# Optimization experiments

Hardware: AMD Instinct MI355X
Metric: run time of the kernel (lower is better)

The kernel has to match this reference:

```python
import jax, jax.numpy as jnp
import numpy as np

D_MODEL = 1024
N_HEADS = 16
D_HEAD = D_MODEL // N_HEADS
SCALE = D_HEAD ** -0.5


def setup_inputs() -> dict:
    key = jax.random.key(0)
    ks = jax.random.split(key, 9)
    s = 0.02
    x = jax.random.normal(ks[0], (2, 2048, D_MODEL), dtype=jnp.float32)
    Wq = jax.random.normal(ks[1], (D_MODEL, D_MODEL), dtype=jnp.float32) * s
    Wk = jax.random.normal(ks[2], (D_MODEL, D_MODEL), dtype=jnp.float32) * s
    Wv = jax.random.normal(ks[3], (D_MODEL, D_MODEL), dtype=jnp.float32) * s
    Wo = jax.random.normal(ks[4], (D_MODEL, D_MODEL), dtype=jnp.float32) * s
    bq = jax.random.normal(ks[5], (D_MODEL,), dtype=jnp.float32) * s
    bk = jax.random.normal(ks[6], (D_MODEL,), dtype=jnp.float32) * s
    bv = jax.random.normal(ks[7], (D_MODEL,), dtype=jnp.float32) * s
    bo = jax.random.normal(ks[8], (D_MODEL,), dtype=jnp.float32) * s
    return {"x": x, "Wq": Wq, "bq": bq, "Wk": Wk, "bk": bk,
            "Wv": Wv, "bv": bv, "Wo": Wo, "bo": bo}


def reference(x, Wq, bq, Wk, bk, Wv, bv, Wo, bo):
    B, S, _ = x.shape
    # torch nn.Linear: y = x @ W.T + b
    def proj(W, b):
        h = jnp.einsum('bsd,ed->bse', x, W) + b
        return h.reshape(B, S, N_HEADS, D_HEAD).transpose(0, 2, 1, 3)  # [B,H,S,Dh]
    Q = proj(Wq, bq)
    K = proj(Wk, bk)
    V = proj(Wv, bv)
    # chunked QK^T softmax over full K == full attention (no mask, dropout=0)
    scores = jnp.einsum('bhqd,bhkd->bhqk', Q, K) * SCALE  # [B,H,S,S]
    attn = jax.nn.softmax(scores, axis=-1)
    out = jnp.einsum('bhqk,bhkd->bhqd', attn, V)
    out = out.transpose(0, 2, 1, 3).reshape(B, S, D_MODEL)
    return jnp.einsum('bsd,ed->bse', out, Wo) + bo
```

## Files before the change

kernel.cpp:

```cpp
#include <hip/hip_runtime.h>
#include <cstdint>
#include <cstddef>


typedef unsigned short u16;
typedef unsigned int u32;
typedef __bf16 bf16x8 __attribute__((ext_vector_type(8)));
typedef float f32x4 __attribute__((ext_vector_type(4)));

#define GLOAD_LDS16(gp, lp)                                                            \
  __builtin_amdgcn_global_load_lds((const __attribute__((address_space(1))) void*)(gp),\
                                   (__attribute__((address_space(3))) void*)(lp),      \
                                   16, 0, 0)

__device__ __forceinline__ u16 f2bf(float f) {
  unsigned u = __builtin_bit_cast(unsigned, f);
  u = u + 0x7fffu + ((u >> 16) & 1u);
  return (u16)(u >> 16);
}

__device__ __forceinline__ u32 pack_bf2(float a, float b) {
  u32 ua = __builtin_bit_cast(u32, a) + 0x8000u;
  u32 ub = __builtin_bit_cast(u32, b) + 0x8000u;
  return __builtin_amdgcn_perm(ub, ua, 0x07060302u);
}

#define QSCALE 0.1803368801111204f

__global__ void cvt_all(const float* __restrict__ x,
                        const float* __restrict__ wq, const float* __restrict__ wk,
                        const float* __restrict__ wv, const float* __restrict__ wo,
                        u16* __restrict__ xb, u16* __restrict__ wqb,
                        u16* __restrict__ wkb, u16* __restrict__ wvb,
                        u16* __restrict__ wob) {
  int bx = blockIdx.x;
  const float* s; u16* d; int off;
  if (bx < 2048)      { s = x;  d = xb;  off = bx; }
  else if (bx < 2560) { s = wq; d = wqb; off = bx - 2048; }
  else if (bx < 3072) { s = wk; d = wkb; off = bx - 2560; }
  else if (bx < 3584) { s = wv; d = wvb; off = bx - 3072; }
  else                { s = wo; d = wob; off = bx - 3584; }
  int i = off * 2048 + threadIdx.x * 8;
  float4 a = *(const float4*)(s + i);
  float4 b = *(const float4*)(s + i + 4);
  uint4 o;
  o.x = f2bf(a.x) | ((u32)f2bf(a.y) << 16);
  o.y = f2bf(a.z) | ((u32)f2bf(a.w) << 16);
  o.z = f2bf(b.x) | ((u32)f2bf(b.y) << 16);
  o.w = f2bf(b.z) | ((u32)f2bf(b.w) << 16);
  *(uint4*)(d + i) = o;
}

template <int MODE>
__global__ __launch_bounds__(256, 3) void gemm_mfma(
    const u16* __restrict__ A,
    const u16* __restrict__ W0, const u16* __restrict__ W1, const u16* __restrict__ W2,
    const float* __restrict__ b0, const float* __restrict__ b1, const float* __restrict__ b2,
    u16* __restrict__ o0, u16* __restrict__ o1, u16* __restrict__ o2,
    float* __restrict__ oF)
{
  __shared__ __align__(16) u16 As[128 * 64];
  __shared__ __align__(16) u16 Bs[128 * 64];

  const int tid = threadIdx.x;
  const int w = tid >> 6, l = tid & 63;
  const int lane = l & 15, quad = l >> 4;
  const int wm = w >> 1, wn = w & 1;
  const int m0 = blockIdx.y * 128;
  const int n0g = blockIdx.x * 128;

  const int src = (MODE == 0) ? (n0g >> 10) : 0;
  const u16* Wsel = (MODE == 0) ? (src == 0 ? W0 : (src == 1 ? W1 : W2)) : W0;
  const float* bsel = (MODE == 0) ? (src == 0 ? b0 : (src == 1 ? b1 : b2)) : b0;
  const int n_base = (MODE == 0) ? (n0g & 1023) : n0g;

  const int c8 = ((l & 7) ^ (l >> 3)) * 8;

  f32x4 acc[4][4] = {};

  for (int kt = 0; kt < 1024; kt += 64) {
    __syncthreads();
    const u16* Ag = A + (size_t)m0 * 1024 + kt;
    const u16* Bg = Wsel + (size_t)n_base * 1024 + kt;
    #pragma unroll
    for (int i = 0; i < 4; ++i) {
      int rr = w * 32 + i * 8;
      GLOAD_LDS16(Ag + (size_t)(rr + (l >> 3)) * 1024 + c8, As + rr * 64);
      GLOAD_LDS16(Bg + (size_t)(rr + (l >> 3)) * 1024 + c8, Bs + rr * 64);
    }
    __syncthreads();

    bf16x8 af[4][2], bf[4][2];
    #pragma unroll
    for (int mf = 0; mf < 4; ++mf)
      #pragma unroll
      for (int ks = 0; ks < 2; ++ks) {
        af[mf][ks] = *(const bf16x8*)((const char*)As +
            (wm * 64 + mf * 16 + lane) * 128 + (((ks * 4 + quad) ^ (lane & 7)) * 16));
        bf[mf][ks] = *(const bf16x8*)((const char*)Bs +
            (wn * 64 + mf * 16 + lane) * 128 + (((ks * 4 + quad) ^ (lane & 7)) * 16));
      }
    #pragma unroll
    for (int ks = 0; ks < 2; ++ks)
      #pragma unroll
      for (int mf = 0; mf < 4; ++mf)
        #pragma unroll
        for (int nf = 0; nf < 4; ++nf)
          acc[mf][nf] = __builtin_amdgcn_mfma_f32_16x16x32_bf16(
              af[mf][ks], bf[nf][ks], acc[mf][nf], 0, 0, 0);
  }

  float bb[4];
  #pragma unroll
  for (int nf = 0; nf < 4; ++nf) bb[nf] = bsel[n_base + wn * 64 + nf * 16 + lane];

  u16* osel = (MODE == 0) ? (src == 0 ? o0 : (src == 1 ? o1 : o2)) : o0;

  #pragma unroll
  for (int mf = 0; mf < 4; ++mf) {
    int mb = m0 + wm * 64 + mf * 16 + quad * 4;
    #pragma unroll
    for (int nf = 0; nf < 4; ++nf) {
      int n_l = wn * 64 + nf * 16 + lane;
      if (MODE == 0 && src == 2) {
        float v0 = acc[mf][nf][0] + bb[nf];
        float v1 = acc[mf][nf][1] + bb[nf];
        float v2 = acc[mf][nf][2] + bb[nf];
        float v3 = acc[mf][nf][3] + bb[nf];
        int bi = mb >> 11, s = mb & 2047;
        int n_in = n_base + n_l;
        int h = n_in >> 6, dh = n_in & 63;
        uint2 pk = make_uint2(pack_bf2(v0, v1), pack_bf2(v2, v3));
        *(uint2*)(osel + (((size_t)(bi * 16 + h) * 64 + dh) * 2048 + s)) = pk;
      } else {
        #pragma unroll
        for (int r = 0; r < 4; ++r) {
          float v = acc[mf][nf][r] + bb[nf];
          int m = mb + r;
          if (MODE == 0) {
            if (src == 0) v *= QSCALE;
            int bi = m >> 11, s = m & 2047;
            int n_in = n_base + n_l;
            int h = n_in >> 6, dh = n_in & 63;
            osel[(((size_t)(bi * 16 + h) * 2048 + s) << 6) + dh] = f2bf(v);
          } else {
            oF[(size_t)m * 1024 + n0g + n_l] = v;
          }
        }
      }
    }
  }
}

__global__ __launch_bounds__(256, 2) void attn_mfma(
    const u16* __restrict__ Qg_, const u16* __restrict__ Kg_,
    const u16* __restrict__ VTg_, u16* __restrict__ Og)
{
  __shared__ __align__(16) u16 Ks[2][64 * 64];
  __shared__ __align__(16) u16 Vs[2][64 * 64];
  __shared__ __align__(16) u16 Ps[4][32 * 64];

  const int tid = threadIdx.x;
  const int w = tid >> 6, l = tid & 63;
  const int lane = l & 15, quad = l >> 4;
  const int bh = blockIdx.y;
  const int q0 = blockIdx.x * 128;

  const u16* Qg = Qg_ + ((size_t)bh * 2048 + q0) * 64;
  const u16* Kg = Kg_ + (size_t)bh * 2048 * 64;
  const u16* VTg = VTg_ + (size_t)bh * 64 * 2048;

  const int c8 = ((l & 7) ^ (l >> 3)) * 8;
  const int lrow = l >> 3;

  bf16x8 bq[2][2];
  #pragma unroll
  for (int qf = 0; qf < 2; ++qf)
    #pragma unroll
    for (int ks = 0; ks < 2; ++ks)
      bq[qf][ks] = *(const bf16x8*)(Qg +
          (size_t)(w * 32 + qf * 16 + lane) * 64 + ks * 32 + quad * 8);

  #pragma unroll
  for (int i = 0; i < 2; ++i) {
    int rr = w * 16 + i * 8;
    GLOAD_LDS16(Kg + (size_t)(rr + lrow) * 64 + c8, Ks[0] + rr * 64);
    GLOAD_LDS16(VTg + (size_t)(rr + lrow) * 2048 + c8, Vs[0] + rr * 64);
  }

  f32x4 oa[2][4] = {};
  float lsum[2] = {0.f, 0.f};
  u16* Pw = Ps[w];

  for (int kt = 0; kt < 32; ++kt) {
    const int buf = kt & 1;
    __syncthreads();
    if (kt < 31) {
      const u16* Kt = Kg + (size_t)(kt + 1) * 64 * 64;
      const u16* Vt = VTg + (size_t)(kt + 1) * 64;
      #pragma unroll
      for (int i = 0; i < 2; ++i) {
        int rr = w * 16 + i * 8;
        GLOAD_LDS16(Kt + (size_t)(rr + lrow) * 64 + c8, Ks[buf ^ 1] + rr * 64);
        GLOAD_LDS16(Vt + (size_t)(rr + lrow) * 2048 + c8, Vs[buf ^ 1] + rr * 64);
      }
    }

    f32x4 sa[4][2] = {};
    #pragma unroll
    for (int ks = 0; ks < 2; ++ks)
      #pragma unroll
      for (int kf = 0; kf < 4; ++kf) {
        bf16x8 ak = *(const bf16x8*)((const char*)Ks[buf] +
            (kf * 16 + lane) * 128 + (((ks * 4 + quad) ^ (lane & 7)) * 16));
        #pragma unroll
        for (int qf = 0; qf < 2; ++qf)
          sa[kf][qf] = __builtin_amdgcn_mfma_f32_16x16x32_bf16(
              ak, bq[qf][ks], sa[kf][qf], 0, 0, 0);
      }

    #pragma unroll
    for (int qf = 0; qf < 2; ++qf) {
      int qrow = qf * 16 + lane;
      #pragma unroll
      for (int kf = 0; kf < 4; ++kf) {
        float p0 = __builtin_amdgcn_exp2f(sa[kf][qf][0]);
        float p1 = __builtin_amdgcn_exp2f(sa[kf][qf][1]);
        float p2 = __builtin_amdgcn_exp2f(sa[kf][qf][2]);
        float p3 = __builtin_amdgcn_exp2f(sa[kf][qf][3]);
        lsum[qf] += (p0 + p1) + (p2 + p3);
        int c = kf * 2 + (quad >> 1);
        *(uint2*)((char*)Pw + qrow * 128 + ((c ^ (lane & 7)) * 16) + (quad & 1) * 8)
            = make_uint2(pack_bf2(p0, p1), pack_bf2(p2, p3));
      }
    }

    #pragma unroll
    for (int ks = 0; ks < 2; ++ks) {
      bf16x8 bv[4];
      #pragma unroll
      for (int df = 0; df < 4; ++df)
        bv[df] = *(const bf16x8*)((const char*)Vs[buf] +
            (df * 16 + lane) * 128 + (((ks * 4 + quad) ^ (lane & 7)) * 16));
      #pragma unroll
      for (int qf = 0; qf < 2; ++qf) {
        bf16x8 ap = *(const bf16x8*)((const char*)Pw +
            (qf * 16 + lane) * 128 + (((ks * 4 + quad) ^ (lane & 7)) * 16));
        #pragma unroll
        for (int df = 0; df < 4; ++df)
          oa[qf][df] = __builtin_amdgcn_mfma_f32_16x16x32_bf16(
              ap, bv[df], oa[qf][df], 0, 0, 0);
      }
    }
  }

  #pragma unroll
  for (int qf = 0; qf < 2; ++qf) {
    lsum[qf] += __shfl_xor(lsum[qf], 16);
    lsum[qf] += __shfl_xor(lsum[qf], 32);
  }
  #pragma unroll
  for (int qf = 0; qf < 2; ++qf)
    #pragma unroll
    for (int r = 0; r < 4; ++r) {
      float inv = 1.0f / __shfl(lsum[qf], quad * 4 + r, 16);
      int qg = q0 + w * 32 + qf * 16 + quad * 4 + r;
      size_t base = ((size_t)(bh >> 4) * 2048 + qg) * 1024 + (bh & 15) * 64;
      #pragma unroll
      for (int df = 0; df < 4; ++df)
        Og[base + df * 16 + lane] = f2bf(oa[qf][df][r] * inv);
    }
}

extern "C" void kernel_launch(void* const* d_in, const int* in_sizes, int n_in,
                              void* d_out, int out_size, void* d_ws, size_t ws_size,
                              hipStream_t stream)
{
  (void)in_sizes; (void)n_in; (void)out_size; (void)ws_size;
  const float* x  = (const float*)d_in[0];
  const float* Wq = (const float*)d_in[1];
  const float* bq = (const float*)d_in[2];
  const float* Wk = (const float*)d_in[3];
  const float* bk = (const float*)d_in[4];
  const float* Wv = (const float*)d_in[5];
  const float* bv = (const float*)d_in[6];
  const float* Wo = (const float*)d_in[7];
  const float* bo = (const float*)d_in[8];
  float* y = (float*)d_out;

  const size_t NM = (size_t)4096 * 1024;
  u16* xb  = (u16*)d_ws;
  u16* wqb = xb + NM;
  u16* wkb = wqb + 1024 * 1024;
  u16* wvb = wkb + 1024 * 1024;
  u16* wob = wvb + 1024 * 1024;
  u16* Qb  = wob + 1024 * 1024;
  u16* Kb  = Qb + NM;
  u16* VTb = Kb + NM;
  u16* AOb = VTb + NM;

  cvt_all<<<4096, 256, 0, stream>>>(x, Wq, Wk, Wv, Wo, xb, wqb, wkb, wvb, wob);

  gemm_mfma<0><<<dim3(24, 32), 256, 0, stream>>>(
      xb, wqb, wkb, wvb, bq, bk, bv, Qb, Kb, VTb, nullptr);

  attn_mfma<<<dim3(16, 32), 256, 0, stream>>>(Qb, Kb, VTb, AOb);

  gemm_mfma<1><<<dim3(8, 32), 256, 0, stream>>>(
      AOb, wob, nullptr, nullptr, bo, nullptr, nullptr,
      nullptr, nullptr, nullptr, y);
}
```

Measured before the change: 191.6 us.

## Load K/V tiles directly into registers per wave, drop shared K/V staging

```diff
diff --git a/kernel.cpp b/kernel.cpp
--- a/kernel.cpp
+++ b/kernel.cpp
@@ -156,120 +156,118 @@
     const u16* __restrict__ Qg_, const u16* __restrict__ Kg_,
     const u16* __restrict__ VTg_, u16* __restrict__ Og)
 {
-  __shared__ __align__(16) u16 Ks[2][64 * 64];
-  __shared__ __align__(16) u16 Vs[2][64 * 64];
-  __shared__ __align__(16) u16 Ps[4][32 * 64];
+  __shared__ __align__(16) u16 Ps[4][32 * 72];
 
   const int tid = threadIdx.x;
   const int w = tid >> 6, l = tid & 63;
   const int lane = l & 15, quad = l >> 4;
   const int bh = blockIdx.y;
-  const int q0 = blockIdx.x * 128;
+  const int q0 = blockIdx.x * 128 + w * 32;
 
   const u16* Qg = Qg_ + ((size_t)bh * 2048 + q0) * 64;
-  const u16* Kg = Kg_ + (size_t)bh * 2048 * 64;
-  const u16* VTg = VTg_ + (size_t)bh * 64 * 2048;
-
-  const int c8 = ((l & 7) ^ (l >> 3)) * 8;
-  const int lrow = l >> 3;
+  const u16* Kg = Kg_ + (size_t)bh * 2048 * 64 + (size_t)lane * 64 + quad * 8;
+  const u16* VTg = VTg_ + (size_t)bh * 64 * 2048 + (size_t)lane * 2048 + quad * 8;
 
   bf16x8 bq[2][2];
   #pragma unroll
   for (int qf = 0; qf < 2; ++qf)
     #pragma unroll
     for (int ks = 0; ks < 2; ++ks)
-      bq[qf][ks] = *(const bf16x8*)(Qg +
-          (size_t)(w * 32 + qf * 16 + lane) * 64 + ks * 32 + quad * 8);
-
-  #pragma unroll
-  for (int i = 0; i < 2; ++i) {
-    int rr = w * 16 + i * 8;
-    GLOAD_LDS16(Kg + (size_t)(rr + lrow) * 64 + c8, Ks[0] + rr * 64);
-    GLOAD_LDS16(VTg + (size_t)(rr + lrow) * 2048 + c8, Vs[0] + rr * 64);
-  }
+      bq[qf][ks] = *(const bf16x8*)(Qg + (size_t)(qf * 16 + lane) * 64 + ks * 32 + quad * 8);
 
   f32x4 oa[2][4] = {};
   float lsum[2] = {0.f, 0.f};
   u16* Pw = Ps[w];
 
-  for (int kt = 0; kt < 32; ++kt) {
-    const int buf = kt & 1;
-    __syncthreads();
-    if (kt < 31) {
-      const u16* Kt = Kg + (size_t)(kt + 1) * 64 * 64;
-      const u16* Vt = VTg + (size_t)(kt + 1) * 64;
-      #pragma unroll
-      for (int i = 0; i < 2; ++i) {
-        int rr = w * 16 + i * 8;
-        GLOAD_LDS16(Kt + (size_t)(rr + lrow) * 64 + c8, Ks[buf ^ 1] + rr * 64);
-        GLOAD_LDS16(Vt + (size_t)(rr + lrow) * 2048 + c8, Vs[buf ^ 1] + rr * 64);
-      }
-    }
-
-    f32x4 sa[4][2] = {};
+  bf16x8 akA[4][2], akB[4][2];
+  #pragma unroll
+  for (int kf = 0; kf < 4; ++kf)
     #pragma unroll
     for (int ks = 0; ks < 2; ++ks)
-      #pragma unroll
-      for (int kf = 0; kf < 4; ++kf) {
-        bf16x8 ak = *(const bf16x8*)((const char*)Ks[buf] +
-            (kf * 16 + lane) * 128 + (((ks * 4 + quad) ^ (lane & 7)) * 16));
-        #pragma unroll
-        for (int qf = 0; qf < 2; ++qf)
-          sa[kf][qf] = __builtin_amdgcn_mfma_f32_16x16x32_bf16(
-              ak, bq[qf][ks], sa[kf][qf], 0, 0, 0);
-      }
-
-    #pragma unroll
-    for (int qf = 0; qf < 2; ++qf) {
-      int qrow = qf * 16 + lane;
-      #pragma unroll
-      for (int kf = 0; kf < 4; ++kf) {
-        float p0 = __builtin_amdgcn_exp2f(sa[kf][qf][0]);
-        float p1 = __builtin_amdgcn_exp2f(sa[kf][qf][1]);
-        float p2 = __builtin_amdgcn_exp2f(sa[kf][qf][2]);
-        float p3 = __builtin_amdgcn_exp2f(sa[kf][qf][3]);
-        lsum[qf] += (p0 + p1) + (p2 + p3);
-        int c = kf * 2 + (quad >> 1);
-        *(uint2*)((char*)Pw + qrow * 128 + ((c ^ (lane & 7)) * 16) + (quad & 1) * 8)
-            = make_uint2(pack_bf2(p0, p1), pack_bf2(p2, p3));
-      }
-    }
-
-    #pragma unroll
-    for (int ks = 0; ks < 2; ++ks) {
-      bf16x8 bv[4];
-      #pragma unroll
-      for (int df = 0; df < 4; ++df)
-        bv[df] = *(const bf16x8*)((const char*)Vs[buf] +
-            (df * 16 + lane) * 128 + (((ks * 4 + quad) ^ (lane & 7)) * 16));
-      #pragma unroll
-      for (int qf = 0; qf < 2; ++qf) {
-        bf16x8 ap = *(const bf16x8*)((const char*)Pw +
-            (qf * 16 + lane) * 128 + (((ks * 4 + quad) ^ (lane & 7)) * 16));
-        #pragma unroll
-        for (int df = 0; df < 4; ++df)
-          oa[qf][df] = __builtin_amdgcn_mfma_f32_16x16x32_bf16(
-              ap, bv[df], oa[qf][df], 0, 0, 0);
-      }
-    }
-  }
+      akA[kf][ks] = *(const bf16x8*)(Kg + (size_t)(kf * 16) * 64 + ks * 32);
+
+#define TILE_BODY(AKC, AKN, KT)                                                 \
+  {                                                                             \
+    const int kt_ = (KT);                                                       \
+           \
+    bf16x8 bv[4][2];                                                            \
+    _Pragma("unroll") for (int df = 0; df < 4; ++df)                            \
+      _Pragma("unroll") for (int ks = 0; ks < 2; ++ks)                          \
+        bv[df][ks] = *(const bf16x8*)(VTg + (size_t)df * 32768 + kt_ * 64 + ks * 32); \
+         \
+    f32x4 sa[4][2] = {};                                                        \
+    _Pragma("unroll") for (int ks = 0; ks < 2; ++ks)                            \
+      _Pragma("unroll") for (int kf = 0; kf < 4; ++kf)                          \
+        _Pragma("unroll") for (int qf = 0; qf < 2; ++qf)                        \
+          sa[kf][qf] = __builtin_amdgcn_mfma_f32_16x16x32_bf16(                 \
+              AKC[kf][ks], bq[qf][ks], sa[kf][qf], 0, 0, 0);                    \
+                   \
+    {                                                                           \
+      int ktn = kt_ + 1; if (ktn > 31) ktn = 31;                                \
+      _Pragma("unroll") for (int kf = 0; kf < 4; ++kf)                          \
+        _Pragma("unroll") for (int ks = 0; ks < 2; ++ks)                        \
+          AKN[kf][ks] = *(const bf16x8*)(Kg + (size_t)(ktn * 64 + kf * 16) * 64 + ks * 32); \
+    }                                                                           \
+      \
+    _Pragma("unroll") for (int qf = 0; qf < 2; ++qf) {                          \
+      int qrow = qf * 16 + lane;                                                \
+      _Pragma("unroll") for (int kf = 0; kf < 4; ++kf) {                        \
+        float p0 = __builtin_amdgcn_exp2f(sa[kf][qf][0]);                       \
+        float p1 = __builtin_amdgcn_exp2f(sa[kf][qf][1]);                       \
+        float p2 = __builtin_amdgcn_exp2f(sa[kf][qf][2]);                       \
+        float p3 = __builtin_amdgcn_exp2f(sa[kf][qf][3]);                       \
+        lsum[qf] += (p0 + p1) + (p2 + p3);                                      \
+        int c = kf * 2 + (quad >> 1);                                           \
+        *(uint2*)((char*)Pw + qrow * 144 + ((c ^ (lane & 7)) * 16) + (quad & 1) * 8) \
+            = make_uint2(pack_bf2(p0, p1), pack_bf2(p2, p3));                   \
+      }                                                                         \
+    }                                                                           \
+                      \
+    _Pragma("unroll") for (int ks = 0; ks < 2; ++ks) {                          \
+      bf16x8 ap[2];                                                             \
+      _Pragma("unroll") for (int qf = 0; qf < 2; ++qf)                          \
+        ap[qf] = *(const bf16x8*)((const char*)Pw +                             \
+            (qf * 16 + lane) * 144 + (((ks * 4 + quad) ^ (lane & 7)) * 16));    \
+      _Pragma("unroll") for (int qf = 0; qf < 2; ++qf)                          \
+        _Pragma("unroll") for (int df = 0; df < 4; ++df)                        \
+          oa[qf][df] = __builtin_amdgcn_mfma_f32_16x16x32_bf16(                 \
+              ap[qf], bv[df][ks], oa[qf][df], 0, 0, 0);                         \
+    }                                                                           \
+  }
+
+  for (int kt = 0; kt < 32; kt += 2) {
+    TILE_BODY(akA, akB, kt);
+    TILE_BODY(akB, akA, kt + 1);
+  }
+#undef TILE_BODY
 
   #pragma unroll
   for (int qf = 0; qf < 2; ++qf) {
     lsum[qf] += __shfl_xor(lsum[qf], 16);
     lsum[qf] += __shfl_xor(lsum[qf], 32);
   }
-  #pragma unroll
-  for (int qf = 0; qf < 2; ++qf)
+
+  #pragma unroll
+  for (int qf = 0; qf < 2; ++qf) {
     #pragma unroll
     for (int r = 0; r < 4; ++r) {
       float inv = 1.0f / __shfl(lsum[qf], quad * 4 + r, 16);
-      int qg = q0 + w * 32 + qf * 16 + quad * 4 + r;
-      size_t base = ((size_t)(bh >> 4) * 2048 + qg) * 1024 + (bh & 15) * 64;
       #pragma unroll
       for (int df = 0; df < 4; ++df)
-        Og[base + df * 16 + lane] = f2bf(oa[qf][df][r] * inv);
+        Pw[(qf * 16 + quad * 4 + r) * 72 + df * 16 + lane] =
+            f2bf(oa[qf][df][r] * inv);
     }
+  }
+  {
+    const int b = bh >> 4, h = bh & 15;
+    u16* Obase = Og + ((size_t)b * 2048 + q0) * 1024 + h * 64;
+    const int rr = l >> 3, cc = l & 7;
+    #pragma unroll
+    for (int i = 0; i < 4; ++i) {
+      uint4 t = *(const uint4*)((const char*)Pw + (i * 8 + rr) * 144 + cc * 16);
+      *(uint4*)(Obase + (size_t)(i * 8 + rr) * 1024 + cc * 8) = t;
+    }
+  }
 }
 
 extern "C" void kernel_launch(void* const* d_in, const int* in_sizes, int n_in,
```

Measured after the change: 260.4 us. 36.0% more time.

## Split attention block across 8 waves with 16 query rows each

Applied to the files above, without the earlier changes.

```diff
diff --git a/kernel.cpp b/kernel.cpp
--- a/kernel.cpp
+++ b/kernel.cpp
@@ -131,7 +131,7 @@
         int n_in = n_base + n_l;
         int h = n_in >> 6, dh = n_in & 63;
         uint2 pk = make_uint2(pack_bf2(v0, v1), pack_bf2(v2, v3));
-        *(uint2*)(osel + (((size_t)(bi * 16 + h) * 64 + dh) * 2048 + s)) = pk;
+        *(uint2*)(o2 + (((size_t)(bi * 16 + h) * 64 + dh) * 2048 + s)) = pk;
       } else {
         #pragma unroll
         for (int r = 0; r < 4; ++r) {
@@ -152,13 +152,13 @@
   }
 }
 
-__global__ __launch_bounds__(256, 2) void attn_mfma(
+__global__ __launch_bounds__(512, 4) void attn_mfma(
     const u16* __restrict__ Qg_, const u16* __restrict__ Kg_,
     const u16* __restrict__ VTg_, u16* __restrict__ Og)
 {
   __shared__ __align__(16) u16 Ks[2][64 * 64];
   __shared__ __align__(16) u16 Vs[2][64 * 64];
-  __shared__ __align__(16) u16 Ps[4][32 * 64];
+  __shared__ __align__(16) u16 Ps[8][16 * 64];
 
   const int tid = threadIdx.x;
   const int w = tid >> 6, l = tid & 63;
@@ -172,104 +172,79 @@
 
   const int c8 = ((l & 7) ^ (l >> 3)) * 8;
   const int lrow = l >> 3;
-
-  bf16x8 bq[2][2];
-  #pragma unroll
-  for (int qf = 0; qf < 2; ++qf)
-    #pragma unroll
-    for (int ks = 0; ks < 2; ++ks)
-      bq[qf][ks] = *(const bf16x8*)(Qg +
-          (size_t)(w * 32 + qf * 16 + lane) * 64 + ks * 32 + quad * 8);
-
-  #pragma unroll
-  for (int i = 0; i < 2; ++i) {
-    int rr = w * 16 + i * 8;
-    GLOAD_LDS16(Kg + (size_t)(rr + lrow) * 64 + c8, Ks[0] + rr * 64);
-    GLOAD_LDS16(VTg + (size_t)(rr + lrow) * 2048 + c8, Vs[0] + rr * 64);
-  }
-
-  f32x4 oa[2][4] = {};
-  float lsum[2] = {0.f, 0.f};
+  const int rr = w * 8;
+
+  bf16x8 bq[2];
+  #pragma unroll
+  for (int ks = 0; ks < 2; ++ks)
+    bq[ks] = *(const bf16x8*)(Qg +
+        (size_t)(w * 16 + lane) * 64 + ks * 32 + quad * 8);
+
+  GLOAD_LDS16(Kg + (size_t)(rr + lrow) * 64 + c8, Ks[0] + rr * 64);
+  GLOAD_LDS16(VTg + (size_t)(rr + lrow) * 2048 + c8, Vs[0] + rr * 64);
+
+  f32x4 oa[4] = {};
+  float lsum = 0.f;
   u16* Pw = Ps[w];
 
   for (int kt = 0; kt < 32; ++kt) {
     const int buf = kt & 1;
     __syncthreads();
+
     if (kt < 31) {
-      const u16* Kt = Kg + (size_t)(kt + 1) * 64 * 64;
-      const u16* Vt = VTg + (size_t)(kt + 1) * 64;
-      #pragma unroll
-      for (int i = 0; i < 2; ++i) {
-        int rr = w * 16 + i * 8;
-        GLOAD_LDS16(Kt + (size_t)(rr + lrow) * 64 + c8, Ks[buf ^ 1] + rr * 64);
-        GLOAD_LDS16(Vt + (size_t)(rr + lrow) * 2048 + c8, Vs[buf ^ 1] + rr * 64);
-      }
-    }
-
-    f32x4 sa[4][2] = {};
+      GLOAD_LDS16(Kg + (size_t)((kt + 1) * 64 + rr + lrow) * 64 + c8,
+                  Ks[buf ^ 1] + rr * 64);
+      GLOAD_LDS16(VTg + (size_t)(rr + lrow) * 2048 + (kt + 1) * 64 + c8,
+                  Vs[buf ^ 1] + rr * 64);
+    }
+
+    f32x4 sa[4] = {};
     #pragma unroll
     for (int ks = 0; ks < 2; ++ks)
       #pragma unroll
       for (int kf = 0; kf < 4; ++kf) {
         bf16x8 ak = *(const bf16x8*)((const char*)Ks[buf] +
             (kf * 16 + lane) * 128 + (((ks * 4 + quad) ^ (lane & 7)) * 16));
-        #pragma unroll
-        for (int qf = 0; qf < 2; ++qf)
-          sa[kf][qf] = __builtin_amdgcn_mfma_f32_16x16x32_bf16(
-              ak, bq[qf][ks], sa[kf][qf], 0, 0, 0);
-      }
-
-    #pragma unroll
-    for (int qf = 0; qf < 2; ++qf) {
-      int qrow = qf * 16 + lane;
-      #pragma unroll
-      for (int kf = 0; kf < 4; ++kf) {
-        float p0 = __builtin_amdgcn_exp2f(sa[kf][qf][0]);
-        float p1 = __builtin_amdgcn_exp2f(sa[kf][qf][1]);
-        float p2 = __builtin_amdgcn_exp2f(sa[kf][qf][2]);
-        float p3 = __builtin_amdgcn_exp2f(sa[kf][qf][3]);
-        lsum[qf] += (p0 + p1) + (p2 + p3);
-        int c = kf * 2 + (quad >> 1);
-        *(uint2*)((char*)Pw + qrow * 128 + ((c ^ (lane & 7)) * 16) + (quad & 1) * 8)
-            = make_uint2(pack_bf2(p0, p1), pack_bf2(p2, p3));
-      }
+        sa[kf] = __builtin_amdgcn_mfma_f32_16x16x32_bf16(ak, bq[ks], sa[kf], 0, 0, 0);
+      }
+
+    #pragma unroll
+    for (int kf = 0; kf < 4; ++kf) {
+      float p0 = __builtin_amdgcn_exp2f(sa[kf][0]);
+      float p1 = __builtin_amdgcn_exp2f(sa[kf][1]);
+      float p2 = __builtin_amdgcn_exp2f(sa[kf][2]);
+      float p3 = __builtin_amdgcn_exp2f(sa[kf][3]);
+      lsum += (p0 + p1) + (p2 + p3);
+      int c = kf * 2 + (quad >> 1);
+      *(uint2*)((char*)Pw + lane * 128 + ((c ^ (lane & 7)) * 16) + (quad & 1) * 8)
+          = make_uint2(pack_bf2(p0, p1), pack_bf2(p2, p3));
     }
 
     #pragma unroll
     for (int ks = 0; ks < 2; ++ks) {
-      bf16x8 bv[4];
-      #pragma unroll
-      for (int df = 0; df < 4; ++df)
-        bv[df] = *(const bf16x8*)((const char*)Vs[buf] +
+      bf16x8 ap = *(const bf16x8*)((const char*)Pw +
+          lane * 128 + (((ks * 4 + quad) ^ (lane & 7)) * 16));
+      #pragma unroll
+      for (int df = 0; df < 4; ++df) {
+        bf16x8 bv = *(const bf16x8*)((const char*)Vs[buf] +
             (df * 16 + lane) * 128 + (((ks * 4 + quad) ^ (lane & 7)) * 16));
-      #pragma unroll
-      for (int qf = 0; qf < 2; ++qf) {
-        bf16x8 ap = *(const bf16x8*)((const char*)Pw +
-            (qf * 16 + lane) * 128 + (((ks * 4 + quad) ^ (lane & 7)) * 16));
-        #pragma unroll
-        for (int df = 0; df < 4; ++df)
-          oa[qf][df] = __builtin_amdgcn_mfma_f32_16x16x32_bf16(
-              ap, bv[df], oa[qf][df], 0, 0, 0);
-      }
-    }
-  }
-
-  #pragma unroll
-  for (int qf = 0; qf < 2; ++qf) {
-    lsum[qf] += __shfl_xor(lsum[qf], 16);
-    lsum[qf] += __shfl_xor(lsum[qf], 32);
-  }
-  #pragma unroll
-  for (int qf = 0; qf < 2; ++qf)
-    #pragma unroll
-    for (int r = 0; r < 4; ++r) {
-      float inv = 1.0f / __shfl(lsum[qf], quad * 4 + r, 16);
-      int qg = q0 + w * 32 + qf * 16 + quad * 4 + r;
-      size_t base = ((size_t)(bh >> 4) * 2048 + qg) * 1024 + (bh & 15) * 64;
-      #pragma unroll
-      for (int df = 0; df < 4; ++df)
-        Og[base + df * 16 + lane] = f2bf(oa[qf][df][r] * inv);
-    }
+        oa[df] = __builtin_amdgcn_mfma_f32_16x16x32_bf16(ap, bv, oa[df], 0, 0, 0);
+      }
+    }
+  }
+
+  lsum += __shfl_xor(lsum, 16);
+  lsum += __shfl_xor(lsum, 32);
+
+  #pragma unroll
+  for (int r = 0; r < 4; ++r) {
+    float inv = 1.0f / __shfl(lsum, quad * 4 + r, 16);
+    int qg = q0 + w * 16 + quad * 4 + r;
+    size_t base = ((size_t)(bh >> 4) * 2048 + qg) * 1024 + (bh & 15) * 64;
+    #pragma unroll
+    for (int df = 0; df < 4; ++df)
+      Og[base + df * 16 + lane] = f2bf(oa[df][r] * inv);
+  }
 }
 
 extern "C" void kernel_launch(void* const* d_in, const int* in_sizes, int n_in,
@@ -304,7 +279,7 @@
   gemm_mfma<0><<<dim3(24, 32), 256, 0, stream>>>(
       xb, wqb, wkb, wvb, bq, bk, bv, Qb, Kb, VTb, nullptr);
 
-  attn_mfma<<<dim3(16, 32), 256, 0, stream>>>(Qb, Kb, VTb, AOb);
+  attn_mfma<<<dim3(16, 32), 512, 0, stream>>>(Qb, Kb, VTb, AOb);
 
   gemm_mfma<1><<<dim3(8, 32), 256, 0, stream>>>(
       AOb, wob, nullptr, nullptr, bo, nullptr, nullptr,
```

Result: no change. 191.2 us (-0.2%).
